# Kernel tuning notes

Hardware: AMD Instinct MI355X
Metric: run time of the kernel (lower is better)

The kernel has to match this reference:

```python
import jax, jax.numpy as jnp
import numpy as np

NUM_CLASSES = 4096
SCALE_FACTOR = 1.0


def setup_inputs() -> dict:
    key = jax.random.key(0)
    k1, k2 = jax.random.split(key)
    logits = jax.random.normal(k1, (8192, NUM_CLASSES), dtype=jnp.float32)
    targets = jax.random.randint(k2, (8192,), 0, NUM_CLASSES, dtype=jnp.int64)
    return {"logits": logits, "targets": targets}


def reference(logits, targets):
    # valid = targets < num_classes (all valid by construction, kept for faithfulness)
    valid = (targets < NUM_CLASSES)
    n_valid = jnp.sum(valid.astype(jnp.float32))

    pred = jax.nn.softmax(logits, axis=-1)                 # (B, C)
    pred_cdf = jnp.cumsum(pred, axis=-1)                   # (B, C)
    # one-hot target CDF is a step function: 1 where class index >= target
    classes = jnp.arange(NUM_CLASSES)                      # (C,)
    target_cdf = (classes[None, :] >= targets[:, None]).astype(pred_cdf.dtype)

    w1 = jnp.sum(jnp.abs(pred_cdf - target_cdf), axis=-1) / NUM_CLASSES  # (B,)
    w1 = w1 * SCALE_FACTOR
    # reduction='mean' over valid samples; returns 0.0 if none valid
    loss = jnp.where(n_valid > 0,
                     jnp.sum(jnp.where(valid, w1, 0.0)) / jnp.maximum(n_valid, 1.0),
                     0.0)
    return loss
```

## Files before the change

kernel.cpp:

```cpp
#include <hip/hip_runtime.h>

#define NUM_CLASSES 4096
#define ROWS 8192

__global__ __launch_bounds__(256) void w1_row_kernel(const float* __restrict__ logits,
                                                     const int* __restrict__ targets,
                                                     float* __restrict__ row_w1) {
    const int r = blockIdx.x;
    const int tid = threadIdx.x;
    const float4* rowp = reinterpret_cast<const float4*>(logits + (size_t)r * NUM_CLASSES);

    const float4 v0 = rowp[tid];
    const float4 v1 = rowp[256 + tid];
    const float4 v2 = rowp[512 + tid];
    const float4 v3 = rowp[768 + tid];
    const float t = (float)targets[r];

    float m = fmaxf(fmaxf(fmaxf(v0.x, v0.y), fmaxf(v0.z, v0.w)),
                    fmaxf(fmaxf(v1.x, v1.y), fmaxf(v1.z, v1.w)));
    m = fmaxf(m, fmaxf(fmaxf(fmaxf(v2.x, v2.y), fmaxf(v2.z, v2.w)),
                       fmaxf(fmaxf(v3.x, v3.y), fmaxf(v3.z, v3.w))));
    #pragma unroll
    for (int off = 1; off < 64; off <<= 1) m = fmaxf(m, __shfl_xor(m, off, 64));

    __shared__ float smax[4];
    __shared__ float ssum[4];
    __shared__ float swsum[4];
    const int wave = tid >> 6;
    if ((tid & 63) == 0) smax[wave] = m;
    __syncthreads();
    m = fmaxf(fmaxf(smax[0], smax[1]), fmaxf(smax[2], smax[3]));

    const float c = (float)(tid * 4) - t;
    float s0 = 0.f, s1 = 0.f, w0 = 0.f, w1 = 0.f;

#define W1_ACC(vv, base, S, W)                                              \
    {                                                                       \
        const float e0 = __expf(vv.x - m);                                  \
        const float e1 = __expf(vv.y - m);                                  \
        const float e2 = __expf(vv.z - m);                                  \
        const float e3 = __expf(vv.w - m);                                  \
        S += (e0 + e1) + (e2 + e3);                                         \
        W += e0 * fabsf(c + (base + 0.f)) + e1 * fabsf(c + (base + 1.f))   \
           + e2 * fabsf(c + (base + 2.f)) + e3 * fabsf(c + (base + 3.f)); \
    }

    W1_ACC(v0, 0.f, s0, w0)
    W1_ACC(v1, 1024.f, s1, w1)
    W1_ACC(v2, 2048.f, s0, w0)
    W1_ACC(v3, 3072.f, s1, w1)
#undef W1_ACC

    float s = s0 + s1;
    float w = w0 + w1;

    #pragma unroll
    for (int off = 1; off < 64; off <<= 1) {
        s += __shfl_xor(s, off, 64);
        w += __shfl_xor(w, off, 64);
    }
    if ((tid & 63) == 0) { ssum[wave] = s; swsum[wave] = w; }
    __syncthreads();

    if (tid == 0) {
        s = (ssum[0] + ssum[1]) + (ssum[2] + ssum[3]);
        w = (swsum[0] + swsum[1]) + (swsum[2] + swsum[3]);
        row_w1[r] = (w / s) * (1.0f / NUM_CLASSES);
    }
}

__global__ __launch_bounds__(256) void w1_reduce_kernel(const float* __restrict__ row_w1,
                                                        float* __restrict__ out) {
    const int tid = threadIdx.x;
    const float4* p = reinterpret_cast<const float4*>(row_w1);
    float acc = 0.0f;
    #pragma unroll
    for (int k = 0; k < 8; ++k) {
        const float4 v = p[k * 256 + tid];
        acc += (v.x + v.y) + (v.z + v.w);
    }

    #pragma unroll
    for (int off = 1; off < 64; off <<= 1) acc += __shfl_xor(acc, off, 64);

    __shared__ float sa[4];
    if ((tid & 63) == 0) sa[tid >> 6] = acc;
    __syncthreads();

    if (tid == 0) {
        out[0] = ((sa[0] + sa[1]) + (sa[2] + sa[3])) * (1.0f / ROWS);
    }
}

extern "C" void kernel_launch(void* const* d_in, const int* in_sizes, int n_in,
                              void* d_out, int out_size, void* d_ws, size_t ws_size,
                              hipStream_t stream) {
    const float* logits = (const float*)d_in[0];
    const int* targets = (const int*)d_in[1];
    float* out = (float*)d_out;
    float* row_w1 = (float*)d_ws;

    w1_row_kernel<<<ROWS, 256, 0, stream>>>(logits, targets, row_w1);
    w1_reduce_kernel<<<1, 256, 0, stream>>>(row_w1, out);
}
```

Baseline: 27.46 us.

## Assign one wavefront per row to drop block-level syncs and shared memory

Each 64-lane wavefront now handles a whole row, loading 16 float4 per lane, and each block covers four rows. The two __syncthreads and the LDS cross-wave reductions go away because all reductions stay within a wave. In exchange each lane holds 64 floats in registers, which may lower occupancy and give less latency hiding per row, and there are fewer, larger blocks.

```diff
diff --git a/kernel.cpp b/kernel.cpp
--- a/kernel.cpp
+++ b/kernel.cpp
@@ -6,51 +6,53 @@
 __global__ __launch_bounds__(256) void w1_row_kernel(const float* __restrict__ logits,
                                                      const int* __restrict__ targets,
                                                      float* __restrict__ row_w1) {
-    const int r = blockIdx.x;
     const int tid = threadIdx.x;
+    const int lane = tid & 63;
+    const int wave = tid >> 6;
+    const int r = blockIdx.x * 4 + wave;
     const float4* rowp = reinterpret_cast<const float4*>(logits + (size_t)r * NUM_CLASSES);
 
-    const float4 v0 = rowp[tid];
-    const float4 v1 = rowp[256 + tid];
-    const float4 v2 = rowp[512 + tid];
-    const float4 v3 = rowp[768 + tid];
+    float4 v[16];
+    #pragma unroll
+    for (int k = 0; k < 16; ++k) v[k] = rowp[k * 64 + lane];
     const float t = (float)targets[r];
 
-    float m = fmaxf(fmaxf(fmaxf(v0.x, v0.y), fmaxf(v0.z, v0.w)),
-                    fmaxf(fmaxf(v1.x, v1.y), fmaxf(v1.z, v1.w)));
-    m = fmaxf(m, fmaxf(fmaxf(fmaxf(v2.x, v2.y), fmaxf(v2.z, v2.w)),
-                       fmaxf(fmaxf(v3.x, v3.y), fmaxf(v3.z, v3.w))));
+    float ma = fmaxf(fmaxf(v[0].x, v[0].y), fmaxf(v[0].z, v[0].w));
+    float mb = fmaxf(fmaxf(v[1].x, v[1].y), fmaxf(v[1].z, v[1].w));
+    #pragma unroll
+    for (int k = 2; k < 16; k += 2) {
+        ma = fmaxf(ma, fmaxf(fmaxf(v[k].x, v[k].y), fmaxf(v[k].z, v[k].w)));
+        mb = fmaxf(mb, fmaxf(fmaxf(v[k + 1].x, v[k + 1].y), fmaxf(v[k + 1].z, v[k + 1].w)));
+    }
+    float m = fmaxf(ma, mb);
     #pragma unroll
     for (int off = 1; off < 64; off <<= 1) m = fmaxf(m, __shfl_xor(m, off, 64));
 
-    __shared__ float smax[4];
-    __shared__ float ssum[4];
-    __shared__ float swsum[4];
-    const int wave = tid >> 6;
-    if ((tid & 63) == 0) smax[wave] = m;
-    __syncthreads();
-    m = fmaxf(fmaxf(smax[0], smax[1]), fmaxf(smax[2], smax[3]));
-
-    const float c = (float)(tid * 4) - t;
+    const float c = (float)(lane * 4) - t;
     float s0 = 0.f, s1 = 0.f, w0 = 0.f, w1 = 0.f;
-
-#define W1_ACC(vv, base, S, W)                                              \
-    {                                                                       \
-        const float e0 = __expf(vv.x - m);                                  \
-        const float e1 = __expf(vv.y - m);                                  \
-        const float e2 = __expf(vv.z - m);                                  \
-        const float e3 = __expf(vv.w - m);                                  \
-        S += (e0 + e1) + (e2 + e3);                                         \
-        W += e0 * fabsf(c + (base + 0.f)) + e1 * fabsf(c + (base + 1.f))   \
-           + e2 * fabsf(c + (base + 2.f)) + e3 * fabsf(c + (base + 3.f)); \
+    #pragma unroll
+    for (int k = 0; k < 16; k += 2) {
+        {
+            const float base = (float)(k * 256);
+            const float e0 = __expf(v[k].x - m);
+            const float e1 = __expf(v[k].y - m);
+            const float e2 = __expf(v[k].z - m);
+            const float e3 = __expf(v[k].w - m);
+            s0 += (e0 + e1) + (e2 + e3);
+            w0 += e0 * fabsf(c + (base + 0.f)) + e1 * fabsf(c + (base + 1.f))
+                + e2 * fabsf(c + (base + 2.f)) + e3 * fabsf(c + (base + 3.f));
+        }
+        {
+            const float base = (float)((k + 1) * 256);
+            const float e0 = __expf(v[k + 1].x - m);
+            const float e1 = __expf(v[k + 1].y - m);
+            const float e2 = __expf(v[k + 1].z - m);
+            const float e3 = __expf(v[k + 1].w - m);
+            s1 += (e0 + e1) + (e2 + e3);
+            w1 += e0 * fabsf(c + (base + 0.f)) + e1 * fabsf(c + (base + 1.f))
+                + e2 * fabsf(c + (base + 2.f)) + e3 * fabsf(c + (base + 3.f));
+        }
     }
-
-    W1_ACC(v0, 0.f, s0, w0)
-    W1_ACC(v1, 1024.f, s1, w1)
-    W1_ACC(v2, 2048.f, s0, w0)
-    W1_ACC(v3, 3072.f, s1, w1)
-#undef W1_ACC
-
     float s = s0 + s1;
     float w = w0 + w1;
 
@@ -59,14 +61,7 @@
         s += __shfl_xor(s, off, 64);
         w += __shfl_xor(w, off, 64);
     }
-    if ((tid & 63) == 0) { ssum[wave] = s; swsum[wave] = w; }
-    __syncthreads();
-
-    if (tid == 0) {
-        s = (ssum[0] + ssum[1]) + (ssum[2] + ssum[3]);
-        w = (swsum[0] + swsum[1]) + (swsum[2] + swsum[3]);
-        row_w1[r] = (w / s) * (1.0f / NUM_CLASSES);
-    }
+    if (lane == 0) row_w1[r] = (w / s) * (1.0f / NUM_CLASSES);
 }
 
 __global__ __launch_bounds__(256) void w1_reduce_kernel(const float* __restrict__ row_w1,
@@ -100,6 +95,6 @@
     float* out = (float*)d_out;
     float* row_w1 = (float*)d_ws;
 
-    w1_row_kernel<<<ROWS, 256, 0, stream>>>(logits, targets, row_w1);
+    w1_row_kernel<<<ROWS / 4, 256, 0, stream>>>(logits, targets, row_w1);
     w1_reduce_kernel<<<1, 256, 0, stream>>>(row_w1, out);
 }
```

Result: slower. 28.16 us (+2.5%).
